# Kernel tuning notes

Measured on AMD Instinct MI355X. Metric: run time of the kernel, lower is better.

The kernel has to match this reference:

```python
import jax, jax.numpy as jnp
import numpy as np


def _forward(q, k, Wq, bq, Wk, bk, Wp, bp, eps=1e-4):
    b, ck, hk, wk, dk = k.shape
    n = hk * wk * dk                      # k sequence length == per-block q tokens
    # k branch: flatten spatial, project 256 -> 32
    kf = jnp.einsum('bci,cd->bid', k.reshape(b, ck, n), Wk) + bk   # (b, n, C)
    k_norm = jnp.linalg.norm(kf, axis=1)                           # (b, C): norm over positions (torch dim=1)
    c = q.shape[1]
    hq, wq, dq = q.shape[2], q.shape[3], q.shape[4]
    Nq = hq * wq * dq
    qf = jnp.einsum('bci,cd->bid', q.reshape(b, c, Nq), Wq) + bq   # (b, Nq, C)
    C = qf.shape[-1]
    Bh, Bw, Bd = hq // hk, wq // wk, dq // dk
    G = Bh * Bw * Bd
    # gather all (h_k, w_k, d_k) blocks: (b, G, n, C) -- replaces triple python loop
    qb = (qf.reshape(b, Bh, hk, Bw, wk, Bd, dk, C)
            .transpose(0, 1, 3, 5, 2, 4, 6, 7)
            .reshape(b, G, n, C))
    q_norm = jnp.linalg.norm(qb, axis=2)                           # (b, G, C): per-channel norm over block positions
    denom = jnp.einsum('bc,bgc->bg', k_norm, q_norm) + eps         # scalar per (batch, block)
    # sim[b,g,j,i] = <kf[b,i,:], qb[b,g,j,:]> / denom  (already in post-permute layout)
    sim = jnp.einsum('bic,bgjc->bgji', kf, qb) / denom[:, :, None, None]
    att = jax.nn.softmax(sim, axis=-1)                             # softmax over k positions i
    out = jnp.einsum('bgji,bgic->bgjc', att, qb)                   # (b, G, n, C)
    # min-max renorm over positions within each block (torch dim=1 of (b,n,C))
    mn = out.min(axis=2, keepdims=True)
    mx = out.max(axis=2, keepdims=True)
    v = (out - mn) / (mx - mn + eps)
    # faithful torch reshape: (b, C, n) row-major reinterpreted as (b, hk, wk, dk, C)
    v = v.transpose(0, 1, 3, 2).reshape(b, Bh, Bw, Bd, hk, wk, dk, C)
    # scatter blocks back to full volume
    v = v.transpose(0, 1, 4, 2, 5, 3, 6, 7).reshape(b, hq, wq, dq, C)
    out = jnp.einsum('bhwdc,ce->bhwde', v, Wp) + bp
    return out.transpose(0, 4, 1, 2, 3)                            # (b, C, hq, wq, dq)


def setup_inputs() -> dict:
    key = jax.random.key(0)
    ks = jax.random.split(key, 8)
    nf = 16
    q = jax.random.normal(ks[0], (2, nf * 2, 32, 32, 32), jnp.float32)
    k = jax.random.normal(ks[1], (2, nf * 16, 8, 8, 8), jnp.float32)
    Wq = jax.random.normal(ks[2], (nf * 2, nf * 2), jnp.float32) * 0.05
    bq = jax.random.normal(ks[3], (nf * 2,), jnp.float32) * 0.05
    Wk = jax.random.normal(ks[4], (nf * 16, nf * 2), jnp.float32) * 0.05
    bk = jax.random.normal(ks[5], (nf * 2,), jnp.float32) * 0.05
    Wp = jax.random.normal(ks[6], (nf * 2, nf * 2), jnp.float32) * 0.05
    bp = jax.random.normal(ks[7], (nf * 2,), jnp.float32) * 0.05
    return {"q": q, "k": k, "Wq": Wq, "bq": bq, "Wk": Wk, "bk": bk, "Wp": Wp, "bp": bp}


def reference(q, k, Wq, bq, Wk, bk, Wp, bp):
    return _forward(q, k, Wq, bq, Wk, bk, Wp, bp)
```

## Files before the change

### kernel.cpp

```cpp
#include <hip/hip_runtime.h>
#include <hip/hip_bf16.h>
#include <cstdint>

typedef __attribute__((ext_vector_type(8))) short bf16x8;
typedef __attribute__((ext_vector_type(4))) float f32x4;

static __device__ __forceinline__ float lo16(uint32_t u){ return __uint_as_float(u << 16); }
static __device__ __forceinline__ float hi16(uint32_t u){ return __uint_as_float(u & 0xffff0000u); }
static __device__ __forceinline__ uint32_t f2bf(float x){
    uint32_t u = __float_as_uint(x);
    return (u + 0x7fffu + ((u >> 16) & 1u)) >> 16;
}
static __device__ __forceinline__ uint32_t pack2(float a, float b){
    return f2bf(a) | (f2bf(b) << 16);
}
static __device__ __forceinline__ uint32_t cvtpk(float a, float b){
    uint32_t r;
    asm("v_cvt_pk_bf16_f32 %0, %1, %2" : "=v"(r) : "v"(a), "v"(b));
    return r;
}
static __device__ __forceinline__ void pl32swap(uint32_t &x, uint32_t &y){
    asm("v_permlane32_swap_b32 %0, %1" : "+v"(x), "+v"(y));
}
static __device__ __forceinline__ void pl16swap(uint32_t &x, uint32_t &y){
    asm("v_permlane16_swap_b32 %0, %1" : "+v"(x), "+v"(y));
}
typedef const __attribute__((address_space(1))) uint32_t* gas_u32p;
typedef __attribute__((address_space(3))) uint32_t* las_u32p;
static __device__ __forceinline__ void gload_lds16(const uint32_t* g, uint32_t* l){
    __builtin_amdgcn_global_load_lds((gas_u32p)g, (las_u32p)l, 16, 0, 0);
}

__global__ __launch_bounds__(1024) void k_pre(const float* __restrict__ q,
    const float* __restrict__ k,
    const float* __restrict__ Wq, const float* __restrict__ bq,
    const float* __restrict__ Wk, const float* __restrict__ bk,
    uint32_t* __restrict__ qb_img, uint32_t* __restrict__ kf_img)
{
    __shared__ float buf[9248];
    int t = threadIdx.x;
    int blk = blockIdx.x;
    if (blk < 256){
        float* Wq_s = buf;
        float* bq_s = buf + 1024;
        float* q_s  = buf + 1056;
        int bg = blk >> 1, h = blk & 1;
        int b = bg >> 6, g = bg & 63;
        int bh = g >> 4, bw = (g >> 2) & 3, bd = g & 3;
        Wq_s[t & 1023] = Wq[t & 1023];
        if (t < 32) bq_s[t] = bq[t];
        const float* qbase = q + (size_t)b * 1048576;
        #pragma unroll
        for (int m = 0; m < 2; ++m){
            int L4 = m*1024 + t;
            int f4 = L4 & 1, iw = (L4 >> 1) & 7, ihl = (L4 >> 4) & 3, c = L4 >> 6;
            const float* src = qbase + c*32768 + (bh*8 + h*4 + ihl)*1024
                             + (bw*8 + iw)*32 + bd*8 + f4*4;
            float4 v = *(const float4*)src;
            *(float4*)&q_s[c*256 + ihl*64 + iw*8 + f4*4] = v;
        }
        __syncthreads();
        int d = t & 31, sub = t >> 5;
        float wq[32];
        #pragma unroll
        for (int c = 0; c < 32; ++c) wq[c] = Wq_s[c*32 + d];
        uint32_t* qb_out = qb_img + (size_t)bg * 8192;
        #pragma unroll
        for (int it = 0; it < 2; ++it){
            int jl = it*128 + sub*4;
            float bb = bq_s[d];
            float a0 = bb, a1 = bb, a2 = bb, a3 = bb;
            #pragma unroll
            for (int c = 0; c < 32; ++c){
                float4 qv = *(const float4*)&q_s[c*256 + jl];
                a0 += qv.x * wq[c];
                a1 += qv.y * wq[c];
                a2 += qv.z * wq[c];
                a3 += qv.w * wq[c];
            }
            int jg = h*256 + jl;
            int grp = ((jg >> 3) ^ (d & 7)) & 63;
            int word = (jg & 7) >> 1;
            uint2 wv;
            wv.x = pack2(a0, a1);
            wv.y = pack2(a2, a3);
            *(uint2*)&qb_out[d*256 + grp*4 + word] = wv;
        }
    } else {
        float* Wk_s = buf;
        float* bk_s = buf + 8192;
        float* red  = buf + 8224;
        for (int L = t; L < 8192; L += 1024) Wk_s[L] = Wk[L];
        if (t < 32) bk_s[t] = bk[t];
        __syncthreads();
        int kb_blk = blk - 256;
        int b = kb_blk >> 7, i0 = (kb_blk & 127) * 4;
        int d = t & 31, sub = t >> 5;
        int i = i0 + (sub >> 3);
        int cp = sub & 7;
        const float* kbp = k + (size_t)b * 131072;
        float acc = 0.f;
        #pragma unroll 8
        for (int cc = 0; cc < 32; ++cc){
            int c = cp*32 + cc;
            acc += kbp[c*512 + i] * Wk_s[c*32 + d];
        }
        red[sub*32 + d] = acc;
        __syncthreads();
        if (t < 128){
            int isel = t >> 5, dd = t & 31;
            float s = bk_s[dd];
            #pragma unroll
            for (int cp2 = 0; cp2 < 8; ++cp2) s += red[(isel*8 + cp2)*32 + dd];
            float sO = __shfl_xor(s, 1, 64);
            if ((dd & 1) == 0){
                int dp = dd >> 1;
                int ii = i0 + isel;
                kf_img[b*8192 + ii*16 + (((dp>>2) ^ (ii&3)) & 3)*4 + (dp&3)] = pack2(s, sO);
            }
        }
    }
}

__global__ __launch_bounds__(512) void k_attn_mfma(const uint32_t* __restrict__ kf_img,
    const uint32_t* __restrict__ qb_img,
    float* __restrict__ oraw, float* __restrict__ mnp, float* __restrict__ mxp)
{
    __shared__ uint32_t kfs32[8192];
    __shared__ uint16_t qbV16[16384];
    __shared__ float statA[32][32];
    __shared__ float statB[16][32];
    __shared__ float statC[16][32];
    __shared__ float mred[8][64];
    __shared__ float vssh[32];
    __shared__ float denom_s;
    int t = threadIdx.x;
    int blk = blockIdx.x;
    int bg = blk >> 2, jq = blk & 3;
    int b = bg >> 6;
    int wave = t >> 6, lane = t & 63;
    {
        const uint32_t* gk = kf_img + b*8192;
        const uint32_t* gq = qb_img + (size_t)bg*8192;
        uint32_t* lq = (uint32_t*)qbV16;
        #pragma unroll
        for (int m = 0; m < 4; ++m){
            int off = wave*1024 + m*256;
            gload_lds16(gk + off + lane*4, kfs32 + off);
        }
        #pragma unroll
        for (int m = 0; m < 4; ++m){
            int off = wave*1024 + m*256;
            gload_lds16(gq + off + lane*4, lq + off);
        }
    }
    __syncthreads();
    {
        int dp = t & 15, ig = t >> 4;
        float lo2 = 0.f, hi2 = 0.f;
        #pragma unroll
        for (int ii = 0; ii < 16; ++ii){
            int i = ig*16 + ii;
            uint32_t u = kfs32[i*16 + (((dp>>2) ^ (i&3)) & 3)*4 + (dp&3)];
            float a = lo16(u), c = hi16(u);
            lo2 += a*a; hi2 += c*c;
        }
        statA[ig][dp*2] = lo2; statA[ig][dp*2+1] = hi2;
    }
    {
        int d = t & 31, ig = t >> 5;
        float q2 = 0.f, vs = 0.f;
        #pragma unroll
        for (int ii = 0; ii < 32; ii += 2){
            int i = ig*32 + ii;
            uint32_t u = *(__shared__ uint32_t*)&qbV16[d*512 + (((i>>3) ^ (d&7)) & 63)*8 + (i&7)];
            float a = lo16(u), c = hi16(u);
            q2 += a*a + c*c; vs += a + c;
        }
        statB[ig][d] = q2; statC[ig][d] = vs;
    }
    __syncthreads();
    if (t < 32){
        float kn = 0.f;
        #pragma unroll
        for (int u = 0; u < 32; ++u) kn += statA[u][t];
        float q2 = 0.f, vs = 0.f;
        #pragma unroll
        for (int u = 0; u < 16; ++u){ q2 += statB[u][t]; vs += statC[u][t]; }
        vssh[t] = vs;
        float dv = sqrtf(kn) * sqrtf(q2);
        dv += __shfl_xor(dv, 1, 64);
        dv += __shfl_xor(dv, 2, 64);
        dv += __shfl_xor(dv, 4, 64);
        dv += __shfl_xor(dv, 8, 64);
        dv += __shfl_xor(dv, 16, 64);
        if (t == 0) denom_s = dv + 1e-4f;
    }
    __syncthreads();
    float rden = 1.0f / denom_s;
    int ln15 = lane & 15, quad = lane >> 4;
    float vs0[4], vs1[4];
    #pragma unroll
    for (int r = 0; r < 4; ++r){
        vs0[r] = vssh[quad*4 + r];
        vs1[r] = vssh[16 + quad*4 + r];
    }
    float* obase = oraw + (size_t)bg * 16384;
    int jloc = jq*128 + wave*16 + ln15;
    union { bf16x8 v; uint16_t u[8]; } afr;
    #pragma unroll
    for (int jj = 0; jj < 8; ++jj){
        int d = quad*8 + jj;
        afr.u[jj] = qbV16[d*512 + (((jloc>>3) ^ (d&7)) & 63)*8 + (jloc&7)];
    }
    f32x4 pv0 = {0.f,0.f,0.f,0.f}, pv1 = {0.f,0.f,0.f,0.f};
    float pdn = 0.f;
    for (int sb = 0; sb < 4; ++sb){
        #pragma unroll
        for (int ch = 0; ch < 4; ++ch){
            int ib = sb*128 + ch*32;
            int i0 = ib + ln15;
            int i1 = i0 + 16;
            bf16x8 k0 = *(__shared__ bf16x8*)&kfs32[i0*16 + ((quad ^ (i0&3)) & 3)*4];
            bf16x8 k1 = *(__shared__ bf16x8*)&kfs32[i1*16 + ((quad ^ (i1&3)) & 3)*4];
            f32x4 z = {0.f,0.f,0.f,0.f};
            f32x4 s0 = __builtin_amdgcn_mfma_f32_16x16x32_bf16(k0, afr.v, z, 0, 0, 0);
            f32x4 s1 = __builtin_amdgcn_mfma_f32_16x16x32_bf16(k1, afr.v, z, 0, 0, 0);
            float e0[4], e1[4];
            #pragma unroll
            for (int r = 0; r < 4; ++r){
                float x = s0[r] * rden;
                e0[r] = x + x*x*(0.5f + x*(1.0f/6.0f));
                pdn += e0[r];
                x = s1[r] * rden;
                e1[r] = x + x*x*(0.5f + x*(1.0f/6.0f));
                pdn += e1[r];
            }
            uint32_t A0 = cvtpk(e0[0], e0[1]);
            uint32_t A1 = cvtpk(e0[2], e0[3]);
            uint32_t B0 = cvtpk(e1[0], e1[1]);
            uint32_t B1 = cvtpk(e1[2], e1[3]);
            pl32swap(A0, B0); pl16swap(A0, B0);
            pl32swap(A1, B1); pl16swap(A1, B1);
            union { bf16x8 v; uint32_t w[4]; } bp;
            bp.w[0] = A0; bp.w[1] = A1; bp.w[2] = B0; bp.w[3] = B1;
            int ig = ib + quad*8;
            int c0 = ln15, c1 = 16 + ln15;
            bf16x8 av0 = *(__shared__ bf16x8*)&qbV16[c0*512 + (((ig>>3) ^ (c0&7)) & 63)*8];
            bf16x8 av1 = *(__shared__ bf16x8*)&qbV16[c1*512 + (((ig>>3) ^ (c1&7)) & 63)*8];
            pv0 = __builtin_amdgcn_mfma_f32_16x16x32_bf16(av0, bp.v, pv0, 0, 0, 0);
            pv1 = __builtin_amdgcn_mfma_f32_16x16x32_bf16(av1, bp.v, pv1, 0, 0, 0);
        }
    }
    pdn += __shfl_xor(pdn, 16, 64);
    pdn += __shfl_xor(pdn, 32, 64);
    float rl = 1.0f / (512.f + pdn);
    float o0[4], o1[4];
    #pragma unroll
    for (int r = 0; r < 4; ++r){
        o0[r] = (vs0[r] + pv0[r]) * rl;
        o1[r] = (vs1[r] + pv1[r]) * rl;
        obase[(quad*4 + r)*512 + jloc]      = o0[r];
        obase[(16 + quad*4 + r)*512 + jloc] = o1[r];
    }
    #pragma unroll
    for (int r = 0; r < 4; ++r){
        float mnA = o0[r], mxA = o0[r], mnB = o1[r], mxB = o1[r];
        #pragma unroll
        for (int off = 1; off < 16; off <<= 1){
            mnA = fminf(mnA, __shfl_xor(mnA, off, 64));
            mxA = fmaxf(mxA, __shfl_xor(mxA, off, 64));
            mnB = fminf(mnB, __shfl_xor(mnB, off, 64));
            mxB = fmaxf(mxB, __shfl_xor(mxB, off, 64));
        }
        if (ln15 == 0){
            mred[wave][quad*4 + r]      = mnA;
            mred[wave][32 + quad*4 + r] = mxA;
            mred[wave][16 + quad*4 + r] = mnB;
            mred[wave][48 + quad*4 + r] = mxB;
        }
    }
    __syncthreads();
    if (t < 32){
        float mn = 3e38f, mx = -3e38f;
        #pragma unroll
        for (int w = 0; w < 8; ++w){
            mn = fminf(mn, mred[w][t]);
            mx = fmaxf(mx, mred[w][32 + t]);
        }
        int slot = (bg*4 + jq)*32 + t;
        mnp[slot] = mn;
        mxp[slot] = mx;
    }
}

__global__ __launch_bounds__(256) void k_proj(const float* __restrict__ oraw,
    const float* __restrict__ mnp, const float* __restrict__ mxp,
    const float* __restrict__ Wp, const float* __restrict__ bp,
    float* __restrict__ out)
{
    __shared__ float Wp_s[1024], bp_s[32];
    __shared__ float sh_v[32][33];
    __shared__ float sh_o[32][33];
    int t = threadIdx.x;
    if (t < 32) bp_s[t] = bp[t];
    for (int L = t; L < 1024; L += 256) Wp_s[L] = Wp[L];
    int blk = blockIdx.x;
    int b = blk >> 10, p0 = (blk & 1023) * 32;
    int c = t & 31, ip0 = t >> 5;
    float vv[4];
    #pragma unroll
    for (int m = 0; m < 4; ++m){
        int p = p0 + m*8 + ip0;
        int h = p >> 10, w = (p >> 5) & 31, dsp = p & 31;
        int f = (h >> 3)*262144 + (w >> 3)*65536 + (dsp >> 3)*16384
              + (h & 7)*2048 + (w & 7)*256 + (dsp & 7)*32;
        int flat = f + c;
        int cidx = b*2048 + (flat >> 9);
        int s0 = ((cidx >> 5) << 7) + (cidx & 31);
        float o  = oraw[(size_t)b*1048576 + flat];
        float mn = fminf(fminf(mnp[s0], mnp[s0 + 32]), fminf(mnp[s0 + 64], mnp[s0 + 96]));
        float mx = fmaxf(fmaxf(mxp[s0], mxp[s0 + 32]), fmaxf(mxp[s0 + 64], mxp[s0 + 96]));
        vv[m] = (o - mn) / (mx - mn + 1e-4f);
    }
    __syncthreads();
    #pragma unroll
    for (int m = 0; m < 4; ++m) sh_v[m*8 + ip0][c] = vv[m];
    __syncthreads();
    #pragma unroll
    for (int m = 0; m < 4; ++m){
        int pos = m*8 + ip0;
        float acc = bp_s[c];
        #pragma unroll
        for (int cc = 0; cc < 32; ++cc)
            acc += sh_v[pos][cc] * Wp_s[cc*32 + c];
        sh_o[pos][c] = acc;
    }
    __syncthreads();
    #pragma unroll
    for (int m = 0; m < 4; ++m){
        int e = m*8 + (t >> 5), pi = t & 31;
        out[((size_t)(b*32 + e) << 15) + p0 + pi] = sh_o[pi][e];
    }
}

extern "C" void kernel_launch(void* const* d_in, const int* in_sizes, int n_in,
                              void* d_out, int out_size, void* d_ws, size_t ws_size,
                              hipStream_t stream)
{
    const float* q  = (const float*)d_in[0];
    const float* k  = (const float*)d_in[1];
    const float* Wq = (const float*)d_in[2];
    const float* bq = (const float*)d_in[3];
    const float* Wk = (const float*)d_in[4];
    const float* bk = (const float*)d_in[5];
    const float* Wp = (const float*)d_in[6];
    const float* bp = (const float*)d_in[7];

    float* base      = (float*)d_ws;
    uint32_t* kf_img = (uint32_t*)base;
    uint32_t* qb_img = (uint32_t*)(base + 16384);
    float* oraw      = base + 1064960;
    float* mnp       = base + 3162112;
    float* mxp       = base + 3178496;
    float* outp      = (float*)d_out;

    hipLaunchKernelGGL(k_pre,       dim3(512),  dim3(1024), 0, stream, q, k, Wq, bq, Wk, bk, qb_img, kf_img);
    hipLaunchKernelGGL(k_attn_mfma, dim3(512),  dim3(512),  0, stream, kf_img, qb_img, oraw, mnp, mxp);
    hipLaunchKernelGGL(k_proj,      dim3(2048), dim3(256),  0, stream, oraw, mnp, mxp, Wp, bp, outp);
}
```

Baseline: 113.1 us.

## Compute norm and sum statistics in projection kernel via atomics; read q directly

The per-channel squared norms of kf and qb and the per-channel sums of qb are now accumulated with atomicAdd in the projection kernel. They are no longer recomputed from bf16 LDS data in every attention block, which removes two reduction passes and two barriers from k_attn_mfma. The q projection also drops its LDS staging of q and Wq and reads them straight from global memory. Statistics now come from fp32 values rather than bf16-rounded ones, a small numeric change. The cost is an extra memset launch and atomic contention, plus 4 attention blocks per group now redundantly loading the same statistics from global memory.

Measured after the change: 154.4 us. 1.37x slower.

```diff
diff --git a/kernel.cpp b/kernel.cpp
--- a/kernel.cpp
+++ b/kernel.cpp
@@ -31,74 +31,62 @@
     __builtin_amdgcn_global_load_lds((gas_u32p)g, (las_u32p)l, 16, 0, 0);
 }
 
-__global__ __launch_bounds__(1024) void k_pre(const float* __restrict__ q,
-    const float* __restrict__ k,
+__global__ __launch_bounds__(1024) void k_pre(const float* __restrict__ qg,
+    const float* __restrict__ kg,
     const float* __restrict__ Wq, const float* __restrict__ bq,
     const float* __restrict__ Wk, const float* __restrict__ bk,
-    uint32_t* __restrict__ qb_img, uint32_t* __restrict__ kf_img)
+    uint32_t* __restrict__ qb_img, uint32_t* __restrict__ kf_img,
+    float* __restrict__ kn2g, float* __restrict__ qn2g, float* __restrict__ vsg)
 {
     __shared__ float buf[9248];
     int t = threadIdx.x;
     int blk = blockIdx.x;
     if (blk < 256){
-        float* Wq_s = buf;
-        float* bq_s = buf + 1024;
-        float* q_s  = buf + 1056;
         int bg = blk >> 1, h = blk & 1;
         int b = bg >> 6, g = bg & 63;
         int bh = g >> 4, bw = (g >> 2) & 3, bd = g & 3;
-        Wq_s[t & 1023] = Wq[t & 1023];
-        if (t < 32) bq_s[t] = bq[t];
-        const float* qbase = q + (size_t)b * 1048576;
-        #pragma unroll
-        for (int m = 0; m < 2; ++m){
-            int L4 = m*1024 + t;
-            int f4 = L4 & 1, iw = (L4 >> 1) & 7, ihl = (L4 >> 4) & 3, c = L4 >> 6;
-            const float* src = qbase + c*32768 + (bh*8 + h*4 + ihl)*1024
-                             + (bw*8 + iw)*32 + bd*8 + f4*4;
-            float4 v = *(const float4*)src;
-            *(float4*)&q_s[c*256 + ihl*64 + iw*8 + f4*4] = v;
-        }
-        __syncthreads();
         int d = t & 31, sub = t >> 5;
+        const float* qbase = qg + (size_t)b * 1048576;
         float wq[32];
         #pragma unroll
-        for (int c = 0; c < 32; ++c) wq[c] = Wq_s[c*32 + d];
+        for (int c = 0; c < 32; ++c) wq[c] = Wq[c*32 + d];
+        float bb = bq[d];
         uint32_t* qb_out = qb_img + (size_t)bg * 8192;
+        float q2 = 0.f, vsum_ = 0.f;
         #pragma unroll
         for (int it = 0; it < 2; ++it){
             int jl = it*128 + sub*4;
-            float bb = bq_s[d];
+            int ihl = jl >> 6, iw = (jl >> 3) & 7, f4 = (jl >> 2) & 1;
+            const float* src = qbase + (bh*8 + h*4 + ihl)*1024
+                             + (bw*8 + iw)*32 + bd*8 + f4*4;
             float a0 = bb, a1 = bb, a2 = bb, a3 = bb;
             #pragma unroll
             for (int c = 0; c < 32; ++c){
-                float4 qv = *(const float4*)&q_s[c*256 + jl];
-                a0 += qv.x * wq[c];
-                a1 += qv.y * wq[c];
-                a2 += qv.z * wq[c];
-                a3 += qv.w * wq[c];
+                float4 qv = *(const float4*)(src + c*32768);
+                a0 += qv.x*wq[c]; a1 += qv.y*wq[c];
+                a2 += qv.z*wq[c]; a3 += qv.w*wq[c];
             }
+            q2 += a0*a0 + a1*a1 + a2*a2 + a3*a3;
+            vsum_ += a0 + a1 + a2 + a3;
             int jg = h*256 + jl;
-            int grp = ((jg >> 3) ^ (d & 7)) & 63;
-            int word = (jg & 7) >> 1;
-            uint2 wv;
-            wv.x = pack2(a0, a1);
-            wv.y = pack2(a2, a3);
+            int grp = ((jg>>3) ^ (d&7)) & 63;
+            int word = (jg&7) >> 1;
+            uint2 wv; wv.x = pack2(a0, a1); wv.y = pack2(a2, a3);
             *(uint2*)&qb_out[d*256 + grp*4 + word] = wv;
         }
+        atomicAdd(&qn2g[bg*32 + d], q2);
+        atomicAdd(&vsg[bg*32 + d], vsum_);
     } else {
         float* Wk_s = buf;
-        float* bk_s = buf + 8192;
-        float* red  = buf + 8224;
+        float* red  = buf + 8192;
         for (int L = t; L < 8192; L += 1024) Wk_s[L] = Wk[L];
-        if (t < 32) bk_s[t] = bk[t];
         __syncthreads();
         int kb_blk = blk - 256;
         int b = kb_blk >> 7, i0 = (kb_blk & 127) * 4;
         int d = t & 31, sub = t >> 5;
         int i = i0 + (sub >> 3);
         int cp = sub & 7;
-        const float* kbp = k + (size_t)b * 131072;
+        const float* kbp = kg + (size_t)b * 131072;
         float acc = 0.f;
         #pragma unroll 8
         for (int cc = 0; cc < 32; ++cc){
@@ -109,9 +97,10 @@
         __syncthreads();
         if (t < 128){
             int isel = t >> 5, dd = t & 31;
-            float s = bk_s[dd];
+            float s = bk[dd];
             #pragma unroll
             for (int cp2 = 0; cp2 < 8; ++cp2) s += red[(isel*8 + cp2)*32 + dd];
+            atomicAdd(&kn2g[b*32 + dd], s*s);
             float sO = __shfl_xor(s, 1, 64);
             if ((dd & 1) == 0){
                 int dp = dd >> 1;
@@ -124,13 +113,12 @@
 
 __global__ __launch_bounds__(512) void k_attn_mfma(const uint32_t* __restrict__ kf_img,
     const uint32_t* __restrict__ qb_img,
+    const float* __restrict__ kn2g, const float* __restrict__ qn2g,
+    const float* __restrict__ vsg,
     float* __restrict__ oraw, float* __restrict__ mnp, float* __restrict__ mxp)
 {
     __shared__ uint32_t kfs32[8192];
     __shared__ uint16_t qbV16[16384];
-    __shared__ float statA[32][32];
-    __shared__ float statB[16][32];
-    __shared__ float statC[16][32];
     __shared__ float mred[8][64];
     __shared__ float vssh[32];
     __shared__ float denom_s;
@@ -154,40 +142,10 @@
             gload_lds16(gq + off + lane*4, lq + off);
         }
     }
-    __syncthreads();
-    {
-        int dp = t & 15, ig = t >> 4;
-        float lo2 = 0.f, hi2 = 0.f;
-        #pragma unroll
-        for (int ii = 0; ii < 16; ++ii){
-            int i = ig*16 + ii;
-            uint32_t u = kfs32[i*16 + (((dp>>2) ^ (i&3)) & 3)*4 + (dp&3)];
-            float a = lo16(u), c = hi16(u);
-            lo2 += a*a; hi2 += c*c;
-        }
-        statA[ig][dp*2] = lo2; statA[ig][dp*2+1] = hi2;
-    }
-    {
-        int d = t & 31, ig = t >> 5;
-        float q2 = 0.f, vs = 0.f;
-        #pragma unroll
-        for (int ii = 0; ii < 32; ii += 2){
-            int i = ig*32 + ii;
-            uint32_t u = *(__shared__ uint32_t*)&qbV16[d*512 + (((i>>3) ^ (d&7)) & 63)*8 + (i&7)];
-            float a = lo16(u), c = hi16(u);
-            q2 += a*a + c*c; vs += a + c;
-        }
-        statB[ig][d] = q2; statC[ig][d] = vs;
-    }
-    __syncthreads();
     if (t < 32){
-        float kn = 0.f;
-        #pragma unroll
-        for (int u = 0; u < 32; ++u) kn += statA[u][t];
-        float q2 = 0.f, vs = 0.f;
-        #pragma unroll
-        for (int u = 0; u < 16; ++u){ q2 += statB[u][t]; vs += statC[u][t]; }
-        vssh[t] = vs;
+        float kn = kn2g[b*32 + t];
+        float q2 = qn2g[bg*32 + t];
+        vssh[t] = vsg[bg*32 + t];
         float dv = sqrtf(kn) * sqrtf(q2);
         dv += __shfl_xor(dv, 1, 64);
         dv += __shfl_xor(dv, 2, 64);
@@ -363,9 +321,15 @@
     float* oraw      = base + 1064960;
     float* mnp       = base + 3162112;
     float* mxp       = base + 3178496;
+    float* kn2g      = base + 3194880;
+    float* qn2g      = base + 3194944;
+    float* vsg       = base + 3199040;
     float* outp      = (float*)d_out;
 
-    hipLaunchKernelGGL(k_pre,       dim3(512),  dim3(1024), 0, stream, q, k, Wq, bq, Wk, bk, qb_img, kf_img);
-    hipLaunchKernelGGL(k_attn_mfma, dim3(512),  dim3(512),  0, stream, kf_img, qb_img, oraw, mnp, mxp);
+    hipMemsetAsync(kn2g, 0, (64 + 4096 + 4096) * sizeof(float), stream);
+    hipLaunchKernelGGL(k_pre,       dim3(512),  dim3(1024), 0, stream, q, k, Wq, bq, Wk, bk,
+                       qb_img, kf_img, kn2g, qn2g, vsg);
+    hipLaunchKernelGGL(k_attn_mfma, dim3(512),  dim3(512),  0, stream, kf_img, qb_img,
+                       kn2g, qn2g, vsg, oraw, mnp, mxp);
     hipLaunchKernelGGL(k_proj,      dim3(2048), dim3(256),  0, stream, oraw, mnp, mxp, Wp, bp, outp);
 }
```

## Fuse attention, min-max renorm and output projection into one kernel

Applied to the files above, without the earlier changes.

Merges the attention kernel and the projection kernel. Each block now handles one (batch, group) across all query positions for half of the channels, so the min-max over positions can be reduced inside the block. The 32x32 projection and the scatter to the output volume then run directly from LDS. This removes the raw-output round trip through global memory, the partial min/max arrays and one kernel launch. In exchange the grid halves to 256 blocks, each wave loops over four query tiles serially, the S=QK part is recomputed once per channel half, and the output stores are less coalesced.

After: 114.1 us. No clear change (+0.9%).

```diff
diff --git a/kernel.cpp b/kernel.cpp
--- a/kernel.cpp
+++ b/kernel.cpp
@@ -122,27 +122,35 @@
     }
 }
 
-__global__ __launch_bounds__(512) void k_attn_mfma(const uint32_t* __restrict__ kf_img,
-    const uint32_t* __restrict__ qb_img,
-    float* __restrict__ oraw, float* __restrict__ mnp, float* __restrict__ mxp)
+__global__ __launch_bounds__(512) void k_attn_half(
+    const uint32_t* __restrict__ kf_img, const uint32_t* __restrict__ qb_img,
+    const float* __restrict__ Wp, const float* __restrict__ bp,
+    float* __restrict__ out)
 {
-    __shared__ uint32_t kfs32[8192];
-    __shared__ uint16_t qbV16[16384];
-    __shared__ float statA[32][32];
-    __shared__ float statB[16][32];
-    __shared__ float statC[16][32];
-    __shared__ float mred[8][64];
+    __shared__ uint32_t IMG[16384];
+    __shared__ float statA[1024];
+    __shared__ float statBC[1056];
+    __shared__ float mred[256];
     __shared__ float vssh[32];
+    __shared__ float mnsh[16], rssh[16];
     __shared__ float denom_s;
+
+    uint32_t* kfs32 = IMG;
+    uint16_t* qbV16 = (uint16_t*)(IMG + 8192);
+    float* v_lds = (float*)IMG;
+
     int t = threadIdx.x;
     int blk = blockIdx.x;
-    int bg = blk >> 2, jq = blk & 3;
-    int b = bg >> 6;
+    int bg = blk >> 1, chalf = blk & 1;
+    int b = bg >> 6, g = bg & 63;
+    int bh = g >> 4, bw = (g >> 2) & 3, bd = g & 3;
     int wave = t >> 6, lane = t & 63;
+    int ln15 = lane & 15, quad = lane >> 4;
+
     {
         const uint32_t* gk = kf_img + b*8192;
         const uint32_t* gq = qb_img + (size_t)bg*8192;
-        uint32_t* lq = (uint32_t*)qbV16;
+        uint32_t* lq = IMG + 8192;
         #pragma unroll
         for (int m = 0; m < 4; ++m){
             int off = wave*1024 + m*256;
@@ -165,7 +173,7 @@
             float a = lo16(u), c = hi16(u);
             lo2 += a*a; hi2 += c*c;
         }
-        statA[ig][dp*2] = lo2; statA[ig][dp*2+1] = hi2;
+        statA[ig*32 + dp*2] = lo2; statA[ig*32 + dp*2 + 1] = hi2;
     }
     {
         int d = t & 31, ig = t >> 5;
@@ -177,16 +185,16 @@
             float a = lo16(u), c = hi16(u);
             q2 += a*a + c*c; vs += a + c;
         }
-        statB[ig][d] = q2; statC[ig][d] = vs;
+        statBC[ig*32 + d] = q2; statBC[512 + ig*32 + d] = vs;
     }
     __syncthreads();
     if (t < 32){
         float kn = 0.f;
         #pragma unroll
-        for (int u = 0; u < 32; ++u) kn += statA[u][t];
+        for (int u = 0; u < 32; ++u) kn += statA[u*32 + t];
         float q2 = 0.f, vs = 0.f;
         #pragma unroll
-        for (int u = 0; u < 16; ++u){ q2 += statB[u][t]; vs += statC[u][t]; }
+        for (int u = 0; u < 16; ++u){ q2 += statBC[u*32 + t]; vs += statBC[512 + u*32 + t]; }
         vssh[t] = vs;
         float dv = sqrtf(kn) * sqrtf(q2);
         dv += __shfl_xor(dv, 1, 64);
@@ -198,149 +206,150 @@
     }
     __syncthreads();
     float rden = 1.0f / denom_s;
-    int ln15 = lane & 15, quad = lane >> 4;
-    float vs0[4], vs1[4];
+    float vs_sel[4];
+    #pragma unroll
+    for (int r = 0; r < 4; ++r)
+        vs_sel[r] = vssh[chalf*16 + quad*4 + r];
+    float oq[4][4];
+    float mn[4], mx[4];
+    #pragma unroll
+    for (int r = 0; r < 4; ++r){ mn[r] = 3e38f; mx[r] = -3e38f; }
+    int crow = chalf*16 + ln15;
+    #pragma unroll
+    for (int jq = 0; jq < 4; ++jq){
+        int jloc = jq*128 + wave*16 + ln15;
+        union { bf16x8 v; uint16_t u[8]; } afr;
+        #pragma unroll
+        for (int jj = 0; jj < 8; ++jj){
+            int d = quad*8 + jj;
+            afr.u[jj] = qbV16[d*512 + (((jloc>>3) ^ (d&7)) & 63)*8 + (jloc&7)];
+        }
+        f32x4 pv = {0.f,0.f,0.f,0.f};
+        float pdn = 0.f;
+        for (int sb = 0; sb < 4; ++sb){
+            #pragma unroll
+            for (int ch = 0; ch < 4; ++ch){
+                int ib = sb*128 + ch*32;
+                int i0 = ib + ln15;
+                int i1 = i0 + 16;
+                bf16x8 k0 = *(__shared__ bf16x8*)&kfs32[i0*16 + ((quad ^ (i0&3)) & 3)*4];
+                bf16x8 k1 = *(__shared__ bf16x8*)&kfs32[i1*16 + ((quad ^ (i1&3)) & 3)*4];
+                f32x4 z = {0.f,0.f,0.f,0.f};
+                f32x4 s0 = __builtin_amdgcn_mfma_f32_16x16x32_bf16(k0, afr.v, z, 0, 0, 0);
+                f32x4 s1 = __builtin_amdgcn_mfma_f32_16x16x32_bf16(k1, afr.v, z, 0, 0, 0);
+                float e0[4], e1[4];
+                #pragma unroll
+                for (int r = 0; r < 4; ++r){
+                    float x = s0[r] * rden;
+                    e0[r] = x + x*x*(0.5f + x*(1.0f/6.0f));
+                    pdn += e0[r];
+                    x = s1[r] * rden;
+                    e1[r] = x + x*x*(0.5f + x*(1.0f/6.0f));
+                    pdn += e1[r];
+                }
+                uint32_t A0 = cvtpk(e0[0], e0[1]);
+                uint32_t A1 = cvtpk(e0[2], e0[3]);
+                uint32_t B0 = cvtpk(e1[0], e1[1]);
+                uint32_t B1 = cvtpk(e1[2], e1[3]);
+                pl32swap(A0, B0); pl16swap(A0, B0);
+                pl32swap(A1, B1); pl16swap(A1, B1);
+                union { bf16x8 v; uint32_t w[4]; } bpv;
+                bpv.w[0] = A0; bpv.w[1] = A1; bpv.w[2] = B0; bpv.w[3] = B1;
+                int ig = ib + quad*8;
+                bf16x8 av = *(__shared__ bf16x8*)&qbV16[crow*512 + (((ig>>3) ^ (crow&7)) & 63)*8];
+                pv = __builtin_amdgcn_mfma_f32_16x16x32_bf16(av, bpv.v, pv, 0, 0, 0);
+            }
+        }
+        pdn += __shfl_xor(pdn, 16, 64);
+        pdn += __shfl_xor(pdn, 32, 64);
+        float rl = 1.0f / (512.f + pdn);
+        #pragma unroll
+        for (int r = 0; r < 4; ++r){
+            float o = (vs_sel[r] + pv[r]) * rl;
+            oq[jq][r] = o;
+            mn[r] = fminf(mn[r], o);
+            mx[r] = fmaxf(mx[r], o);
+        }
+    }
     #pragma unroll
     for (int r = 0; r < 4; ++r){
-        vs0[r] = vssh[quad*4 + r];
-        vs1[r] = vssh[16 + quad*4 + r];
-    }
-    float* obase = oraw + (size_t)bg * 16384;
-    int jloc = jq*128 + wave*16 + ln15;
-    union { bf16x8 v; uint16_t u[8]; } afr;
-    #pragma unroll
-    for (int jj = 0; jj < 8; ++jj){
-        int d = quad*8 + jj;
-        afr.u[jj] = qbV16[d*512 + (((jloc>>3) ^ (d&7)) & 63)*8 + (jloc&7)];
-    }
-    f32x4 pv0 = {0.f,0.f,0.f,0.f}, pv1 = {0.f,0.f,0.f,0.f};
-    float pdn = 0.f;
-    for (int sb = 0; sb < 4; ++sb){
-        #pragma unroll
-        for (int ch = 0; ch < 4; ++ch){
-            int ib = sb*128 + ch*32;
-            int i0 = ib + ln15;
-            int i1 = i0 + 16;
-            bf16x8 k0 = *(__shared__ bf16x8*)&kfs32[i0*16 + ((quad ^ (i0&3)) & 3)*4];
-            bf16x8 k1 = *(__shared__ bf16x8*)&kfs32[i1*16 + ((quad ^ (i1&3)) & 3)*4];
-            f32x4 z = {0.f,0.f,0.f,0.f};
-            f32x4 s0 = __builtin_amdgcn_mfma_f32_16x16x32_bf16(k0, afr.v, z, 0, 0, 0);
-            f32x4 s1 = __builtin_amdgcn_mfma_f32_16x16x32_bf16(k1, afr.v, z, 0, 0, 0);
-            float e0[4], e1[4];
-            #pragma unroll
-            for (int r = 0; r < 4; ++r){
-                float x = s0[r] * rden;
-                e0[r] = x + x*x*(0.5f + x*(1.0f/6.0f));
-                pdn += e0[r];
-                x = s1[r] * rden;
-                e1[r] = x + x*x*(0.5f + x*(1.0f/6.0f));
-                pdn += e1[r];
-            }
-            uint32_t A0 = cvtpk(e0[0], e0[1]);
-            uint32_t A1 = cvtpk(e0[2], e0[3]);
-            uint32_t B0 = cvtpk(e1[0], e1[1]);
-            uint32_t B1 = cvtpk(e1[2], e1[3]);
-            pl32swap(A0, B0); pl16swap(A0, B0);
-            pl32swap(A1, B1); pl16swap(A1, B1);
-            union { bf16x8 v; uint32_t w[4]; } bp;
-            bp.w[0] = A0; bp.w[1] = A1; bp.w[2] = B0; bp.w[3] = B1;
-            int ig = ib + quad*8;
-            int c0 = ln15, c1 = 16 + ln15;
-            bf16x8 av0 = *(__shared__ bf16x8*)&qbV16[c0*512 + (((ig>>3) ^ (c0&7)) & 63)*8];
-            bf16x8 av1 = *(__shared__ bf16x8*)&qbV16[c1*512 + (((ig>>3) ^ (c1&7)) & 63)*8];
-            pv0 = __builtin_amdgcn_mfma_f32_16x16x32_bf16(av0, bp.v, pv0, 0, 0, 0);
-            pv1 = __builtin_amdgcn_mfma_f32_16x16x32_bf16(av1, bp.v, pv1, 0, 0, 0);
-        }
-    }
-    pdn += __shfl_xor(pdn, 16, 64);
-    pdn += __shfl_xor(pdn, 32, 64);
-    float rl = 1.0f / (512.f + pdn);
-    float o0[4], o1[4];
-    #pragma unroll
-    for (int r = 0; r < 4; ++r){
-        o0[r] = (vs0[r] + pv0[r]) * rl;
-        o1[r] = (vs1[r] + pv1[r]) * rl;
-        obase[(quad*4 + r)*512 + jloc]      = o0[r];
-        obase[(16 + quad*4 + r)*512 + jloc] = o1[r];
-    }
-    #pragma unroll
-    for (int r = 0; r < 4; ++r){
-        float mnA = o0[r], mxA = o0[r], mnB = o1[r], mxB = o1[r];
         #pragma unroll
         for (int off = 1; off < 16; off <<= 1){
-            mnA = fminf(mnA, __shfl_xor(mnA, off, 64));
-            mxA = fmaxf(mxA, __shfl_xor(mxA, off, 64));
-            mnB = fminf(mnB, __shfl_xor(mnB, off, 64));
-            mxB = fmaxf(mxB, __shfl_xor(mxB, off, 64));
+            mn[r] = fminf(mn[r], __shfl_xor(mn[r], off, 64));
+            mx[r] = fmaxf(mx[r], __shfl_xor(mx[r], off, 64));
         }
         if (ln15 == 0){
-            mred[wave][quad*4 + r]      = mnA;
-            mred[wave][32 + quad*4 + r] = mxA;
-            mred[wave][16 + quad*4 + r] = mnB;
-            mred[wave][48 + quad*4 + r] = mxB;
-        }
-    }
-    __syncthreads();
-    if (t < 32){
-        float mn = 3e38f, mx = -3e38f;
+            mred[wave*32 + quad*4 + r]      = mn[r];
+            mred[wave*32 + 16 + quad*4 + r] = mx[r];
+        }
+    }
+    __syncthreads();
+    if (t < 16){
+        float m0 = 3e38f, m1 = -3e38f;
         #pragma unroll
         for (int w = 0; w < 8; ++w){
-            mn = fminf(mn, mred[w][t]);
-            mx = fmaxf(mx, mred[w][32 + t]);
-        }
-        int slot = (bg*4 + jq)*32 + t;
-        mnp[slot] = mn;
-        mxp[slot] = mx;
-    }
-}
-
-__global__ __launch_bounds__(256) void k_proj(const float* __restrict__ oraw,
-    const float* __restrict__ mnp, const float* __restrict__ mxp,
-    const float* __restrict__ Wp, const float* __restrict__ bp,
-    float* __restrict__ out)
-{
-    __shared__ float Wp_s[1024], bp_s[32];
-    __shared__ float sh_v[32][33];
-    __shared__ float sh_o[32][33];
-    int t = threadIdx.x;
-    if (t < 32) bp_s[t] = bp[t];
-    for (int L = t; L < 1024; L += 256) Wp_s[L] = Wp[L];
-    int blk = blockIdx.x;
-    int b = blk >> 10, p0 = (blk & 1023) * 32;
-    int c = t & 31, ip0 = t >> 5;
-    float vv[4];
-    #pragma unroll
-    for (int m = 0; m < 4; ++m){
-        int p = p0 + m*8 + ip0;
-        int h = p >> 10, w = (p >> 5) & 31, dsp = p & 31;
-        int f = (h >> 3)*262144 + (w >> 3)*65536 + (dsp >> 3)*16384
-              + (h & 7)*2048 + (w & 7)*256 + (dsp & 7)*32;
-        int flat = f + c;
-        int cidx = b*2048 + (flat >> 9);
-        int s0 = ((cidx >> 5) << 7) + (cidx & 31);
-        float o  = oraw[(size_t)b*1048576 + flat];
-        float mn = fminf(fminf(mnp[s0], mnp[s0 + 32]), fminf(mnp[s0 + 64], mnp[s0 + 96]));
-        float mx = fmaxf(fmaxf(mxp[s0], mxp[s0 + 32]), fmaxf(mxp[s0 + 64], mxp[s0 + 96]));
-        vv[m] = (o - mn) / (mx - mn + 1e-4f);
-    }
-    __syncthreads();
-    #pragma unroll
-    for (int m = 0; m < 4; ++m) sh_v[m*8 + ip0][c] = vv[m];
-    __syncthreads();
-    #pragma unroll
-    for (int m = 0; m < 4; ++m){
-        int pos = m*8 + ip0;
-        float acc = bp_s[c];
-        #pragma unroll
-        for (int cc = 0; cc < 32; ++cc)
-            acc += sh_v[pos][cc] * Wp_s[cc*32 + c];
-        sh_o[pos][c] = acc;
-    }
-    __syncthreads();
-    #pragma unroll
-    for (int m = 0; m < 4; ++m){
-        int e = m*8 + (t >> 5), pi = t & 31;
-        out[((size_t)(b*32 + e) << 15) + p0 + pi] = sh_o[pi][e];
+            m0 = fminf(m0, mred[w*32 + t]);
+            m1 = fmaxf(m1, mred[w*32 + 16 + t]);
+        }
+        mnsh[t] = m0;
+        rssh[t] = 1.0f / (m1 - m0 + 1e-4f);
+    }
+    __syncthreads();
+    {
+        float mnr[4], rsr[4];
+        #pragma unroll
+        for (int r = 0; r < 4; ++r){
+            mnr[r] = mnsh[quad*4 + r];
+            rsr[r] = rssh[quad*4 + r];
+        }
+        #pragma unroll
+        for (int jq = 0; jq < 4; ++jq){
+            int j = jq*128 + wave*16 + ln15;
+            #pragma unroll
+            for (int r = 0; r < 4; ++r)
+                v_lds[(quad*4 + r)*512 + j] = (oq[jq][r] - mnr[r]) * rsr[r];
+        }
+        statA[t] = Wp[t];
+        statA[512 + t] = Wp[512 + t];
+    }
+    __syncthreads();
+    {
+        int e = t & 31;
+        float bpv = bp[e];
+        for (int pass = 0; pass < 8; ++pass){
+            #pragma unroll
+            for (int ii = 0; ii < 2; ++ii){
+                int pl = ii*16 + (t >> 5);
+                int P = pass*32 + pl;
+                int c_v = P >> 4, j_hi = P & 15;
+                const float* vrow = &v_lds[c_v*512 + j_hi*32];
+                float S = bpv;
+                #pragma unroll
+                for (int c4 = 0; c4 < 8; ++c4){
+                    float4 vv4 = *(float4*)&vrow[c4*4];
+                    S += vv4.x * statA[(c4*4    )*32 + e]
+                       + vv4.y * statA[(c4*4 + 1)*32 + e]
+                       + vv4.z * statA[(c4*4 + 2)*32 + e]
+                       + vv4.w * statA[(c4*4 + 3)*32 + e];
+                }
+                statBC[pl*33 + e] = S;
+            }
+            __syncthreads();
+            {
+                int d_low = t & 7, e2 = (t >> 3) & 31, hi2 = t >> 8;
+                #pragma unroll
+                for (int m2 = 0; m2 < 2; ++m2){
+                    int pl = hi2*16 + m2*8 + d_low;
+                    int c_v = pass*2 + hi2;
+                    float val = statBC[pl*33 + e2];
+                    int cg = chalf*16 + c_v;
+                    int hl = cg >> 2, wl = (c_v & 3)*2 + m2;
+                    out[((size_t)(b*32 + e2) << 15)
+                        + (bh*8 + hl)*1024 + (bw*8 + wl)*32 + bd*8 + d_low] = val;
+                }
+            }
+            __syncthreads();
+        }
     }
 }
 
@@ -357,15 +366,12 @@
     const float* Wp = (const float*)d_in[6];
     const float* bp = (const float*)d_in[7];
 
-    float* base      = (float*)d_ws;
-    uint32_t* kf_img = (uint32_t*)base;
-    uint32_t* qb_img = (uint32_t*)(base + 16384);
-    float* oraw      = base + 1064960;
-    float* mnp       = base + 3162112;
-    float* mxp       = base + 3178496;
+    uint32_t* kf_img = (uint32_t*)d_ws;
+    uint32_t* qb_img = (uint32_t*)d_ws + 16384;
     float* outp      = (float*)d_out;
 
-    hipLaunchKernelGGL(k_pre,       dim3(512),  dim3(1024), 0, stream, q, k, Wq, bq, Wk, bk, qb_img, kf_img);
-    hipLaunchKernelGGL(k_attn_mfma, dim3(512),  dim3(512),  0, stream, kf_img, qb_img, oraw, mnp, mxp);
-    hipLaunchKernelGGL(k_proj,      dim3(2048), dim3(256),  0, stream, oraw, mnp, mxp, Wp, bp, outp);
-}
+    hipLaunchKernelGGL(k_pre,       dim3(512), dim3(1024), 0, stream, q, k, Wq, bq, Wk, bk,
+                       qb_img, kf_img);
+    hipLaunchKernelGGL(k_attn_half, dim3(256), dim3(512),  0, stream, kf_img, qb_img,
+                       Wp, bp, outp);
+}
```
